# Optimization experiments

Measured on AMD Instinct MI355X. Metric: run time of the kernel, lower is better.

Reference implementation:

```python
import jax, jax.numpy as jnp
import numpy as np
from jax import lax

N_WIRES = 4
N_OPS = 30
BN_EPS = 1e-5


def _rl_ops():
    # Deterministic stand-in for tq.RandomLayer(n_ops=30): cycle rx/ry/rz/cnot.
    kinds = ['rx', 'ry', 'rz', 'cnot']
    ops, p = [], 0
    for i in range(N_OPS):
        k = kinds[i % 4]
        if k == 'cnot':
            ops.append((k, i % N_WIRES, (i + 1) % N_WIRES))
        else:
            ops.append((k, i % N_WIRES, p))
            p += 1
    return ops, p

RL_OPS, N_RL_PARAMS = _rl_ops()  # 23 rotation params, 7 cnots


def _rx(t):
    c = jnp.cos(t / 2).astype(jnp.complex64)
    s = (-1j * jnp.sin(t / 2).astype(jnp.complex64))
    return jnp.stack([jnp.stack([c, s], -1), jnp.stack([s, c], -1)], -2)


def _ry(t):
    c = jnp.cos(t / 2).astype(jnp.complex64)
    s = jnp.sin(t / 2).astype(jnp.complex64)
    return jnp.stack([jnp.stack([c, -s], -1), jnp.stack([s, c], -1)], -2)


def _rz(t):
    e = jnp.exp((-1j * t / 2).astype(jnp.complex64))
    z = jnp.zeros_like(e)
    return jnp.stack([jnp.stack([e, z], -1), jnp.stack([z, jnp.conj(e)], -1)], -2)


def _apply_1q(state, U, w):
    # state: [B,2,2,2,2]; U: [2,2] (shared) or [B,2,2] (per-sample)
    s = jnp.moveaxis(state, w + 1, -1)
    if U.ndim == 2:
        s = jnp.einsum('ij,b...j->b...i', U, s)
    else:
        s = jnp.einsum('bij,b...j->b...i', U, s)
    return jnp.moveaxis(s, -1, w + 1)


def _apply_cnot(state, c, t):
    s = jnp.moveaxis(state, (c + 1, t + 1), (-2, -1))
    s = s.at[..., 1, :].set(s[..., 1, ::-1])  # flip target where control==1
    return jnp.moveaxis(s, (-2, -1), (c + 1, t + 1))


# PauliZ expectation table: z[k, w] = +/-1 for basis state k on wire w
_ZTAB = np.array([[1.0 - 2.0 * ((k >> (N_WIRES - 1 - w)) & 1) for w in range(N_WIRES)]
                  for k in range(2 ** N_WIRES)], dtype=np.float32)  # [16,4]


def _conv(x, w, b):
    y = lax.conv_general_dilated(x, w, (1, 1), 'SAME',
                                 dimension_numbers=('NCHW', 'OIHW', 'NCHW'))
    return y + b[None, :, None, None]


def _maxpool2(x):
    return lax.reduce_window(x, -jnp.inf, lax.max, (1, 1, 2, 2), (1, 1, 2, 2), 'VALID')


def setup_inputs() -> dict:
    key = jax.random.key(0)
    ks = jax.random.split(key, 8)
    B = 8192
    return {
        'x': jax.random.normal(ks[0], (B, 1, 28, 28), jnp.float32),
        'conv1_w': jax.random.normal(ks[1], (8, 1, 3, 3), jnp.float32) * 0.1,
        'conv1_b': jnp.zeros((8,), jnp.float32),
        'conv2_w': jax.random.normal(ks[2], (16, 8, 3, 3), jnp.float32) * 0.1,
        'conv2_b': jnp.zeros((16,), jnp.float32),
        'fc1_w': jax.random.normal(ks[3], (64, 784), jnp.float32) * 0.05,
        'fc1_b': jnp.zeros((64,), jnp.float32),
        'fc2_w': jax.random.normal(ks[4], (4, 64), jnp.float32) * 0.1,
        'fc2_b': jnp.zeros((4,), jnp.float32),
        'bn_g': jnp.ones((4,), jnp.float32),
        'bn_b': jnp.zeros((4,), jnp.float32),
        'rl_params': jax.random.uniform(ks[5], (N_RL_PARAMS,), jnp.float32,
                                        -np.pi, np.pi),
    }


def reference(x, conv1_w, conv1_b, conv2_w, conv2_b, fc1_w, fc1_b,
              fc2_w, fc2_b, bn_g, bn_b, rl_params):
    B = x.shape[0]
    # CNN backbone: conv -> relu -> pool -> conv -> relu -> pool
    h = _maxpool2(jax.nn.relu(_conv(x, conv1_w, conv1_b)))          # [B,8,14,14]
    h = _maxpool2(jax.nn.relu(_conv(h, conv2_w, conv2_b)))          # [B,16,7,7]
    flat = h.reshape(B, -1)                                         # [B,784]
    h = jax.nn.relu(flat @ fc1_w.T + fc1_b)                         # [B,64]
    feat = h @ fc2_w.T + fc2_b                                      # [B,4]
    # BatchNorm1d (training mode: batch stats, biased variance)
    mean = feat.mean(0)
    var = feat.var(0)
    feat = (feat - mean) / jnp.sqrt(var + BN_EPS) * bn_g + bn_b
    # Quantum state-vector simulation on 4 wires, |0000> start
    state = jnp.zeros((B, 16), jnp.complex64).at[:, 0].set(1.0)
    state = state.reshape(B, 2, 2, 2, 2)
    # Encoder: RX(feat[:, w]) on wire w
    for w in range(N_WIRES):
        state = _apply_1q(state, _rx(feat[:, w]), w)
    # Random layer: 30 sequential gates with fixed trainable params
    gate_fns = {'rx': _rx, 'ry': _ry, 'rz': _rz}
    for kind, w, q in RL_OPS:
        if kind == 'cnot':
            state = _apply_cnot(state, w, q)
        else:
            state = _apply_1q(state, gate_fns[kind](rl_params[q]), w)
    # MeasureAll(PauliZ)
    probs = jnp.abs(state.reshape(B, 16)) ** 2                      # [B,16]
    return probs @ jnp.asarray(_ZTAB)                               # [B,4]
```

## Files before the change

kernel.cpp:

```cpp
#include <hip/hip_runtime.h>


#define B_EPS 1e-5f

typedef float f2 __attribute__((ext_vector_type(2)));

__device__ __forceinline__ f2 sp(float x)          { f2 r; r.x = x; r.y = x; return r; }
__device__ __forceinline__ f2 mk(float a, float b) { f2 r; r.x = a; r.y = b; return r; }
#define PKFMA(a, b, c) __builtin_elementwise_fma(a, b, c)
#define PKMAX(a, b)    __builtin_elementwise_max(a, b)

__device__ __forceinline__ void row_fma(f2* acc, const float* wp, const f2* rv)
{
    #pragma unroll
    for (int j = 0; j < 4; j++) {
        acc[j] = PKFMA(sp(wp[0]), rv[j],     acc[j]);
        acc[j] = PKFMA(sp(wp[1]), rv[j + 1], acc[j]);
        acc[j] = PKFMA(sp(wp[2]), rv[j + 2], acc[j]);
    }
}

__device__ __forceinline__ void load_rv6(f2* rv, const f2* rp)
{
    float4 A = *(const float4*)rp;
    float4 Bv = *(const float4*)(rp + 2);
    float4 Cv = *(const float4*)(rp + 4);
    rv[0] = mk(A.x, A.y);   rv[1] = mk(A.z, A.w);
    rv[2] = mk(Bv.x, Bv.y); rv[3] = mk(Bv.z, Bv.w);
    rv[4] = mk(Cv.x, Cv.y); rv[5] = mk(Cv.z, Cv.w);
}

__global__ void prep_kernel(const float* __restrict__ rl,
                            const float* __restrict__ f1w,
                            const float* __restrict__ c2w,
                            float* __restrict__ Uout,
                            float* __restrict__ wT2,
                            float* __restrict__ w2q,
                            float* __restrict__ stats)
{
    if (blockIdx.x == 0) {
        __shared__ float2 U[16][16];
        int t = threadIdx.x;
        int r = t >> 4, cc = t & 15;
        U[r][cc] = (r == cc) ? make_float2(1.f, 0.f) : make_float2(0.f, 0.f);
        stats[t] = 0.f;
        stats[t + 256] = 0.f;
        for (int i = t; i < 16 * 8 * 12; i += 256) {
            int ci = i / 192, rem = i - ci * 192;
            int c2 = rem / 12, qq = rem - c2 * 12;
            w2q[i] = (qq < 9) ? c2w[c2 * 72 + ci * 9 + qq] : 0.f;
        }
        __syncthreads();
        for (int op = 0; op < 30; op++) {
            int kind = op & 3;
            float2 cur = U[r][cc];
            float2 nv;
            if (kind == 3) {
                float2 part = U[r ^ 8][cc];
                nv = (r & 1) ? part : cur;
            } else {
                int m = 8 >> kind;
                float theta = rl[op - (op >> 2)];
                float ch = cosf(0.5f * theta), sh = sinf(0.5f * theta);
                float2 part = U[r ^ m][cc];
                int br = (r & m) ? 1 : 0;
                float2 gc, gp;
                if (kind == 0)      { gc = make_float2(ch, 0.f);           gp = make_float2(0.f, -sh); }
                else if (kind == 1) { gc = make_float2(ch, 0.f);           gp = make_float2(br ? sh : -sh, 0.f); }
                else                { gc = make_float2(ch, br ? sh : -sh); gp = make_float2(0.f, 0.f); }
                nv.x = gc.x*cur.x - gc.y*cur.y + gp.x*part.x - gp.y*part.y;
                nv.y = gc.x*cur.y + gc.y*cur.x + gp.x*part.y + gp.y*part.x;
            }
            __syncthreads();
            U[r][cc] = nv;
            __syncthreads();
        }
        ((float2*)Uout)[t] = U[r][cc];
    } else {
        int id = (blockIdx.x - 1) * 256 + threadIdx.x;
        if (id < 784 * 64) {
            int k = id >> 6, o = id & 63;
            wT2[(((k >> 2) * 64 + o) << 2) + (k & 3)] = f1w[o * 784 + k];
        }
    }
}

__global__ __launch_bounds__(256) void conv_kernel(
    const float* __restrict__ x,  const float* __restrict__ c1w,
    const float* __restrict__ c1b, const float* __restrict__ w2q,
    const float* __restrict__ c2b, const float* __restrict__ wT2,
    const float* __restrict__ f1b, const float* __restrict__ f2w,
    const float* __restrict__ f2bias, float* __restrict__ feat,
    float* __restrict__ stats)
{
    __shared__ union alignas(16) {
        f2 xin[30 * 32];
        f2 flat[784];
    } u;
    __shared__ union alignas(16) {
        f2 p1[8 * 290];
        struct { f2 part[4][64]; f2 hs[64]; } fc;
    } pu;

    int t = threadIdx.x;
    int w = t >> 6, lane = t & 63;

    int c1 = lane >> 3;
    float wk1[9];
    #pragma unroll
    for (int q = 0; q < 9; q++) wk1[q] = c1w[c1 * 9 + q];
    float bias1 = c1b[c1];

    {
        float4 z = make_float4(0.f, 0.f, 0.f, 0.f);
        float4* xz = (float4*)u.xin;
        for (int i = t; i < 480; i += 256) xz[i] = z;
        float4* pz = (float4*)pu.p1;
        for (int i = t; i < 1160; i += 256) pz[i] = z;
    }
    __syncthreads();

    {
        const float4* xg0 = (const float4*)(x + (size_t)blockIdx.x * 2 * 784);
        const float4* xg1 = xg0 + 196;
        if (t < 196) {
            float4 v0 = xg0[t];
            float4 v1 = xg1[t];
            int p = 4 * t, rr = p / 28, cb = p - rr * 28;
            f2* dst = &u.xin[(rr + 1) * 32 + cb + 3];
            dst[0] = mk(v0.x, v1.x);
            dst[1] = mk(v0.y, v1.y);
            dst[2] = mk(v0.z, v1.z);
            dst[3] = mk(v0.w, v1.w);
        }
    }
    __syncthreads();

    {
        int g = lane & 7;
        if (g < 7) {
            const f2* xb = &u.xin[4 * g + 2];
            f2* pout = &pu.p1[c1 * 290 + 3];
            #pragma unroll 1
            for (int k = 0; k < 4; k++) {
                int i = w + 4 * k;
                if (i > 13) break;
                f2 o_[2][4];
                #pragma unroll
                for (int dr = 0; dr < 2; dr++)
                    #pragma unroll
                    for (int j = 0; j < 4; j++) o_[dr][j] = sp(bias1);
                #pragma unroll
                for (int q = 0; q < 4; q++) {
                    f2 rv[6];
                    load_rv6(rv, xb + (2 * i + q) * 32);
                    if (q < 3)  row_fma(o_[0], &wk1[q * 3], rv);
                    if (q >= 1) row_fma(o_[1], &wk1[(q - 1) * 3], rv);
                }
                #pragma unroll
                for (int jj = 0; jj < 2; jj++) {
                    f2 m = PKMAX(PKMAX(o_[0][2 * jj], o_[0][2 * jj + 1]),
                                 PKMAX(o_[1][2 * jj], o_[1][2 * jj + 1]));
                    pout[(i + 1) * 18 + 2 * g + jj] = PKMAX(m, sp(0.f));
                }
            }
        }
    }
    __syncthreads();

    {
        int c2 = lane >> 2, g2 = lane & 3;
        float bias2 = c2b[c2];
        const float4* wqb = (const float4*)w2q + c2 * 3;
        #pragma unroll 1
        for (int k = 0; k < 2; k++) {
            int i = w + 4 * k;
            if (i > 6) break;
            f2 acc[2][4];
            #pragma unroll
            for (int dr = 0; dr < 2; dr++)
                #pragma unroll
                for (int j = 0; j < 4; j++) acc[dr][j] = sp(bias2);
            float4 wa = wqb[0], wb = wqb[1], wc = wqb[2];
            #pragma unroll 1
            for (int ci = 0; ci < 8; ci++) {
                float wk[9] = {wa.x, wa.y, wa.z, wa.w, wb.x, wb.y, wb.z, wb.w, wc.x};
                if (ci < 7) {
                    wa = wqb[(ci + 1) * 48];
                    wb = wqb[(ci + 1) * 48 + 1];
                    wc = wqb[(ci + 1) * 48 + 2];
                }
                const f2* pc_ = &pu.p1[ci * 290 + (2 * i) * 18 + 4 * g2 + 2];
                #pragma unroll
                for (int q = 0; q < 4; q++) {
                    f2 rv[6];
                    load_rv6(rv, pc_ + q * 18);
                    if (q < 3)  row_fma(acc[0], &wk[q * 3], rv);
                    if (q >= 1) row_fma(acc[1], &wk[(q - 1) * 3], rv);
                }
            }
            #pragma unroll
            for (int jj = 0; jj < 2; jj++) {
                int pc = 2 * g2 + jj;
                if (pc < 7) {
                    f2 m = PKMAX(PKMAX(acc[0][2 * jj], acc[0][2 * jj + 1]),
                                 PKMAX(acc[1][2 * jj], acc[1][2 * jj + 1]));
                    u.flat[c2 * 49 + i * 7 + pc] = PKMAX(m, sp(0.f));
                }
            }
        }
    }
    __syncthreads();

    {
        const f2* fl = u.flat;
        const float4* wp4 = (const float4*)wT2 + lane;
        int g0 = w * 49;
        f2 a0 = sp(0.f), a1 = sp(0.f);
        #pragma unroll 2
        for (int g = g0; g < g0 + 48; g += 2) {
            float4 wv0 = wp4[(size_t)g * 64];
            float4 wv1 = wp4[(size_t)(g + 1) * 64];
            float4 fA = *(const float4*)&fl[4 * g];
            float4 fB = *(const float4*)&fl[4 * g + 2];
            float4 fC = *(const float4*)&fl[4 * g + 4];
            float4 fD = *(const float4*)&fl[4 * g + 6];
            a0 = PKFMA(sp(wv0.x), mk(fA.x, fA.y), a0);
            a0 = PKFMA(sp(wv0.y), mk(fA.z, fA.w), a0);
            a0 = PKFMA(sp(wv0.z), mk(fB.x, fB.y), a0);
            a0 = PKFMA(sp(wv0.w), mk(fB.z, fB.w), a0);
            a1 = PKFMA(sp(wv1.x), mk(fC.x, fC.y), a1);
            a1 = PKFMA(sp(wv1.y), mk(fC.z, fC.w), a1);
            a1 = PKFMA(sp(wv1.z), mk(fD.x, fD.y), a1);
            a1 = PKFMA(sp(wv1.w), mk(fD.z, fD.w), a1);
        }
        {
            int g = g0 + 48;
            float4 wv = wp4[(size_t)g * 64];
            float4 fA = *(const float4*)&fl[4 * g];
            float4 fB = *(const float4*)&fl[4 * g + 2];
            a0 = PKFMA(sp(wv.x), mk(fA.x, fA.y), a0);
            a0 = PKFMA(sp(wv.y), mk(fA.z, fA.w), a0);
            a0 = PKFMA(sp(wv.z), mk(fB.x, fB.y), a0);
            a0 = PKFMA(sp(wv.w), mk(fB.z, fB.w), a0);
        }
        pu.fc.part[w][lane] = a0 + a1;
    }
    __syncthreads();

    if (t < 64) {
        f2 h = pu.fc.part[0][t] + pu.fc.part[1][t]
             + pu.fc.part[2][t] + pu.fc.part[3][t] + sp(f1b[t]);
        pu.fc.hs[t] = PKMAX(h, sp(0.f));
    }
    __syncthreads();

    if (t < 4) {
        int j = t;
        f2 a = sp(f2bias[j]);
        #pragma unroll
        for (int o = 0; o < 64; o++) a = PKFMA(sp(f2w[j * 64 + o]), pu.fc.hs[o], a);
        feat[((size_t)blockIdx.x * 2 + 0) * 4 + j] = a.x;
        feat[((size_t)blockIdx.x * 2 + 1) * 4 + j] = a.y;
        int g = blockIdx.x & 63;
        atomicAdd(&stats[g * 8 + j], a.x + a.y);
        atomicAdd(&stats[g * 8 + 4 + j], a.x * a.x + a.y * a.y);
    }
}

__global__ __launch_bounds__(128) void quantum_kernel(
    const float* __restrict__ feat, const float* __restrict__ Ug,
    const float* __restrict__ stats, const float* __restrict__ bn_g,
    const float* __restrict__ bn_b, float* __restrict__ out, int B)
{
    __shared__ float2 Us[256];
    __shared__ float sm[8];
    int t = threadIdx.x;
    for (int i = t; i < 256; i += 128) Us[i] = ((const float2*)Ug)[i];
    if (t < 8) sm[t] = 0.f;
    __syncthreads();
    {
        float v = stats[t] + stats[t + 128] + stats[t + 256] + stats[t + 384];
        atomicAdd(&sm[t & 7], v);
    }
    __syncthreads();
    int q = t & 3;
    int s = blockIdx.x * 32 + (t >> 2);
    float4 fv = ((const float4*)feat)[s];
    float f[4] = {fv.x, fv.y, fv.z, fv.w};
    float cn[4], sn[4];
    float invB = 1.0f / (float)B;
    #pragma unroll
    for (int w = 0; w < 4; w++) {
        float mean = sm[w] * invB;
        float var  = sm[4 + w] * invB - mean * mean;
        float fh = (f[w] - mean) / sqrtf(var + B_EPS) * bn_g[w] + bn_b[w];
        cn[w] = cosf(0.5f * fh);
        sn[w] = sinf(0.5f * fh);
    }
    float re0[16], im0[16];
    #pragma unroll
    for (int k = 0; k < 16; k++) {
        float mag = ((k & 8) ? sn[0] : cn[0]) * ((k & 4) ? sn[1] : cn[1]) *
                    ((k & 2) ? sn[2] : cn[2]) * ((k & 1) ? sn[3] : cn[3]);
        int m = __popc(k) & 3;
        re0[k] = (m == 0) ? mag : (m == 2) ? -mag : 0.f;
        im0[k] = (m == 1) ? -mag : (m == 3) ? mag : 0.f;
    }
    float o0 = 0.f, o1 = 0.f, o2 = 0.f, o3 = 0.f;
    #pragma unroll
    for (int i = 0; i < 4; i++) {
        int r = q * 4 + i;
        float ar = 0.f, ai = 0.f;
        #pragma unroll
        for (int k = 0; k < 16; k++) {
            float2 uu = Us[r * 16 + k];
            ar += uu.x * re0[k] - uu.y * im0[k];
            ai += uu.x * im0[k] + uu.y * re0[k];
        }
        float p = ar * ar + ai * ai;
        o0 += (r & 8) ? -p : p;
        o1 += (r & 4) ? -p : p;
        o2 += (r & 2) ? -p : p;
        o3 += (r & 1) ? -p : p;
    }
    o0 += __shfl_xor(o0, 1);  o0 += __shfl_xor(o0, 2);
    o1 += __shfl_xor(o1, 1);  o1 += __shfl_xor(o1, 2);
    o2 += __shfl_xor(o2, 1);  o2 += __shfl_xor(o2, 2);
    o3 += __shfl_xor(o3, 1);  o3 += __shfl_xor(o3, 2);
    if (q == 0) {
        float4 ov = {o0, o1, o2, o3};
        ((float4*)out)[s] = ov;
    }
}

extern "C" void kernel_launch(void* const* d_in, const int* in_sizes, int n_in,
                              void* d_out, int out_size, void* d_ws, size_t ws_size,
                              hipStream_t stream)
{
    const float* x   = (const float*)d_in[0];
    const float* c1w = (const float*)d_in[1];
    const float* c1b = (const float*)d_in[2];
    const float* c2w = (const float*)d_in[3];
    const float* c2b = (const float*)d_in[4];
    const float* f1w = (const float*)d_in[5];
    const float* f1b = (const float*)d_in[6];
    const float* f2w = (const float*)d_in[7];
    const float* f2b = (const float*)d_in[8];
    const float* bng = (const float*)d_in[9];
    const float* bnb = (const float*)d_in[10];
    const float* rl  = (const float*)d_in[11];
    float* out = (float*)d_out;

    int B = in_sizes[0] / 784;

    float* wsf   = (float*)d_ws;
    float* feat  = wsf;
    float* wT2   = feat + (size_t)B * 4;
    float* U     = wT2 + 784 * 64;
    float* stats = U + 512;
    float* w2q   = stats + 512;

    prep_kernel<<<197, 256, 0, stream>>>(rl, f1w, c2w, U, wT2, w2q, stats);
    conv_kernel<<<B / 2, 256, 0, stream>>>(x, c1w, c1b, w2q, c2b, wT2,
                                           f1b, f2w, f2b, feat, stats);
    quantum_kernel<<<B / 32, 128, 0, stream>>>(feat, U, stats, bng, bnb, out, B);
}
```

Baseline: 185.7 us.

## Compute two output channels per thread in conv1 and conv2 to reuse input loads

Each thread in conv1 and conv2 now accumulates two output channels from the same loaded input rows. This halves the shared-memory input reads per FMA, and the work is remapped across threads. Conv1 now gives each thread two rows with two channels. Conv2 now uses 224 threads, each covering one row with two channels, and loads its weights directly without prefetching. This raises register pressure and leaves 32 threads idle in conv2.

```diff
diff --git a/kernel.cpp b/kernel.cpp
--- a/kernel.cpp
+++ b/kernel.cpp
@@ -105,11 +105,15 @@
     int t = threadIdx.x;
     int w = t >> 6, lane = t & 63;
 
-    int c1 = lane >> 3;
-    float wk1[9];
-    #pragma unroll
-    for (int q = 0; q < 9; q++) wk1[q] = c1w[c1 * 9 + q];
-    float bias1 = c1b[c1];
+    int r2 = lane >> 5;
+    int p2p = (lane >> 3) & 3;
+    int g  = lane & 7;
+
+    int chA = 2 * p2p, chB = 2 * p2p + 1;
+    float wkA[9], wkB[9];
+    #pragma unroll
+    for (int q = 0; q < 9; q++) { wkA[q] = c1w[chA * 9 + q]; wkB[q] = c1w[chB * 9 + q]; }
+    float biasA = c1b[chA], biasB = c1b[chB];
 
     {
         float4 z = make_float4(0.f, 0.f, 0.f, 0.f);
@@ -126,7 +130,7 @@
         if (t < 196) {
             float4 v0 = xg0[t];
             float4 v1 = xg1[t];
-            int p = 4 * t, rr = p / 28, cb = p - rr * 28;
+            int pp = 4 * t, rr = pp / 28, cb = pp - rr * 28;
             f2* dst = &u.xin[(rr + 1) * 32 + cb + 3];
             dst[0] = mk(v0.x, v1.x);
             dst[1] = mk(v0.y, v1.y);
@@ -137,76 +141,84 @@
     __syncthreads();
 
     {
-        int g = lane & 7;
         if (g < 7) {
             const f2* xb = &u.xin[4 * g + 2];
-            f2* pout = &pu.p1[c1 * 290 + 3];
             #pragma unroll 1
-            for (int k = 0; k < 4; k++) {
-                int i = w + 4 * k;
+            for (int k = 0; k < 2; k++) {
+                int i = w * 2 + r2 + 8 * k;
                 if (i > 13) break;
-                f2 o_[2][4];
+                f2 oA[2][4], oB[2][4];
                 #pragma unroll
                 for (int dr = 0; dr < 2; dr++)
                     #pragma unroll
-                    for (int j = 0; j < 4; j++) o_[dr][j] = sp(bias1);
+                    for (int j = 0; j < 4; j++) { oA[dr][j] = sp(biasA); oB[dr][j] = sp(biasB); }
                 #pragma unroll
                 for (int q = 0; q < 4; q++) {
                     f2 rv[6];
                     load_rv6(rv, xb + (2 * i + q) * 32);
-                    if (q < 3)  row_fma(o_[0], &wk1[q * 3], rv);
-                    if (q >= 1) row_fma(o_[1], &wk1[(q - 1) * 3], rv);
+                    if (q < 3)  { row_fma(oA[0], &wkA[q * 3], rv);
+                                  row_fma(oB[0], &wkB[q * 3], rv); }
+                    if (q >= 1) { row_fma(oA[1], &wkA[(q - 1) * 3], rv);
+                                  row_fma(oB[1], &wkB[(q - 1) * 3], rv); }
                 }
+                f2* poutA = &pu.p1[chA * 290 + 3 + (i + 1) * 18 + 2 * g];
+                f2* poutB = &pu.p1[chB * 290 + 3 + (i + 1) * 18 + 2 * g];
                 #pragma unroll
                 for (int jj = 0; jj < 2; jj++) {
-                    f2 m = PKMAX(PKMAX(o_[0][2 * jj], o_[0][2 * jj + 1]),
-                                 PKMAX(o_[1][2 * jj], o_[1][2 * jj + 1]));
-                    pout[(i + 1) * 18 + 2 * g + jj] = PKMAX(m, sp(0.f));
+                    f2 mA = PKMAX(PKMAX(oA[0][2 * jj], oA[0][2 * jj + 1]),
+                                  PKMAX(oA[1][2 * jj], oA[1][2 * jj + 1]));
+                    f2 mB = PKMAX(PKMAX(oB[0][2 * jj], oB[0][2 * jj + 1]),
+                                  PKMAX(oB[1][2 * jj], oB[1][2 * jj + 1]));
+                    poutA[jj] = PKMAX(mA, sp(0.f));
+                    poutB[jj] = PKMAX(mB, sp(0.f));
                 }
             }
         }
     }
     __syncthreads();
 
-    {
-        int c2 = lane >> 2, g2 = lane & 3;
-        float bias2 = c2b[c2];
-        const float4* wqb = (const float4*)w2q + c2 * 3;
-        #pragma unroll 1
-        for (int k = 0; k < 2; k++) {
-            int i = w + 4 * k;
-            if (i > 6) break;
-            f2 acc[2][4];
+    if (t < 224) {
+        int i3  = t >> 5;
+        int p3  = (t >> 2) & 7;
+        int g2  = t & 3;
+        int cA = 2 * p3, cB = 2 * p3 + 1;
+        const float4* wqA = (const float4*)w2q + cA * 3;
+        const float4* wqB = (const float4*)w2q + cB * 3;
+        f2 accA[2][4], accB[2][4];
+        {
+            float bA = c2b[cA], bB = c2b[cB];
             #pragma unroll
             for (int dr = 0; dr < 2; dr++)
                 #pragma unroll
-                for (int j = 0; j < 4; j++) acc[dr][j] = sp(bias2);
-            float4 wa = wqb[0], wb = wqb[1], wc = wqb[2];
-            #pragma unroll 1
-            for (int ci = 0; ci < 8; ci++) {
-                float wk[9] = {wa.x, wa.y, wa.z, wa.w, wb.x, wb.y, wb.z, wb.w, wc.x};
-                if (ci < 7) {
-                    wa = wqb[(ci + 1) * 48];
-                    wb = wqb[(ci + 1) * 48 + 1];
-                    wc = wqb[(ci + 1) * 48 + 2];
-                }
-                const f2* pc_ = &pu.p1[ci * 290 + (2 * i) * 18 + 4 * g2 + 2];
-                #pragma unroll
-                for (int q = 0; q < 4; q++) {
-                    f2 rv[6];
-                    load_rv6(rv, pc_ + q * 18);
-                    if (q < 3)  row_fma(acc[0], &wk[q * 3], rv);
-                    if (q >= 1) row_fma(acc[1], &wk[(q - 1) * 3], rv);
-                }
+                for (int j = 0; j < 4; j++) { accA[dr][j] = sp(bA); accB[dr][j] = sp(bB); }
+        }
+        #pragma unroll 1
+        for (int ci = 0; ci < 8; ci++) {
+            float4 a0 = wqA[ci * 48], a1 = wqA[ci * 48 + 1], a2 = wqA[ci * 48 + 2];
+            float4 b0 = wqB[ci * 48], b1 = wqB[ci * 48 + 1], b2 = wqB[ci * 48 + 2];
+            float wA[9] = {a0.x, a0.y, a0.z, a0.w, a1.x, a1.y, a1.z, a1.w, a2.x};
+            float wB[9] = {b0.x, b0.y, b0.z, b0.w, b1.x, b1.y, b1.z, b1.w, b2.x};
+            const f2* pc_ = &pu.p1[ci * 290 + (2 * i3) * 18 + 4 * g2 + 2];
+            #pragma unroll
+            for (int q = 0; q < 4; q++) {
+                f2 rv[6];
+                load_rv6(rv, pc_ + q * 18);
+                if (q < 3)  { row_fma(accA[0], &wA[q * 3], rv);
+                              row_fma(accB[0], &wB[q * 3], rv); }
+                if (q >= 1) { row_fma(accA[1], &wA[(q - 1) * 3], rv);
+                              row_fma(accB[1], &wB[(q - 1) * 3], rv); }
             }
-            #pragma unroll
-            for (int jj = 0; jj < 2; jj++) {
-                int pc = 2 * g2 + jj;
-                if (pc < 7) {
-                    f2 m = PKMAX(PKMAX(acc[0][2 * jj], acc[0][2 * jj + 1]),
-                                 PKMAX(acc[1][2 * jj], acc[1][2 * jj + 1]));
-                    u.flat[c2 * 49 + i * 7 + pc] = PKMAX(m, sp(0.f));
-                }
+        }
+        #pragma unroll
+        for (int jj = 0; jj < 2; jj++) {
+            int pc = 2 * g2 + jj;
+            if (pc < 7) {
+                f2 mA = PKMAX(PKMAX(accA[0][2 * jj], accA[0][2 * jj + 1]),
+                              PKMAX(accA[1][2 * jj], accA[1][2 * jj + 1]));
+                f2 mB = PKMAX(PKMAX(accB[0][2 * jj], accB[0][2 * jj + 1]),
+                              PKMAX(accB[1][2 * jj], accB[1][2 * jj + 1]));
+                u.flat[cA * 49 + i3 * 7 + pc] = PKMAX(mA, sp(0.f));
+                u.flat[cB * 49 + i3 * 7 + pc] = PKMAX(mB, sp(0.f));
             }
         }
     }
@@ -218,13 +230,13 @@
         int g0 = w * 49;
         f2 a0 = sp(0.f), a1 = sp(0.f);
         #pragma unroll 2
-        for (int g = g0; g < g0 + 48; g += 2) {
-            float4 wv0 = wp4[(size_t)g * 64];
-            float4 wv1 = wp4[(size_t)(g + 1) * 64];
-            float4 fA = *(const float4*)&fl[4 * g];
-            float4 fB = *(const float4*)&fl[4 * g + 2];
-            float4 fC = *(const float4*)&fl[4 * g + 4];
-            float4 fD = *(const float4*)&fl[4 * g + 6];
+        for (int gg = g0; gg < g0 + 48; gg += 2) {
+            float4 wv0 = wp4[(size_t)gg * 64];
+            float4 wv1 = wp4[(size_t)(gg + 1) * 64];
+            float4 fA = *(const float4*)&fl[4 * gg];
+            float4 fB = *(const float4*)&fl[4 * gg + 2];
+            float4 fC = *(const float4*)&fl[4 * gg + 4];
+            float4 fD = *(const float4*)&fl[4 * gg + 6];
             a0 = PKFMA(sp(wv0.x), mk(fA.x, fA.y), a0);
             a0 = PKFMA(sp(wv0.y), mk(fA.z, fA.w), a0);
             a0 = PKFMA(sp(wv0.z), mk(fB.x, fB.y), a0);
@@ -235,10 +247,10 @@
             a1 = PKFMA(sp(wv1.w), mk(fD.z, fD.w), a1);
         }
         {
-            int g = g0 + 48;
-            float4 wv = wp4[(size_t)g * 64];
-            float4 fA = *(const float4*)&fl[4 * g];
-            float4 fB = *(const float4*)&fl[4 * g + 2];
+            int gg = g0 + 48;
+            float4 wv = wp4[(size_t)gg * 64];
+            float4 fA = *(const float4*)&fl[4 * gg];
+            float4 fB = *(const float4*)&fl[4 * gg + 2];
             a0 = PKFMA(sp(wv.x), mk(fA.x, fA.y), a0);
             a0 = PKFMA(sp(wv.y), mk(fA.z, fA.w), a0);
             a0 = PKFMA(sp(wv.z), mk(fB.x, fB.y), a0);
@@ -262,9 +274,9 @@
         for (int o = 0; o < 64; o++) a = PKFMA(sp(f2w[j * 64 + o]), pu.fc.hs[o], a);
         feat[((size_t)blockIdx.x * 2 + 0) * 4 + j] = a.x;
         feat[((size_t)blockIdx.x * 2 + 1) * 4 + j] = a.y;
-        int g = blockIdx.x & 63;
-        atomicAdd(&stats[g * 8 + j], a.x + a.y);
-        atomicAdd(&stats[g * 8 + 4 + j], a.x * a.x + a.y * a.y);
+        int g2 = blockIdx.x & 63;
+        atomicAdd(&stats[g2 * 8 + j], a.x + a.y);
+        atomicAdd(&stats[g2 * 8 + 4 + j], a.x * a.x + a.y * a.y);
     }
 }
 
@@ -318,11 +330,11 @@
             ar += uu.x * re0[k] - uu.y * im0[k];
             ai += uu.x * im0[k] + uu.y * re0[k];
         }
-        float p = ar * ar + ai * ai;
-        o0 += (r & 8) ? -p : p;
-        o1 += (r & 4) ? -p : p;
-        o2 += (r & 2) ? -p : p;
-        o3 += (r & 1) ? -p : p;
+        float pqr = ar * ar + ai * ai;
+        o0 += (r & 8) ? -pqr : pqr;
+        o1 += (r & 4) ? -pqr : pqr;
+        o2 += (r & 2) ? -pqr : pqr;
+        o3 += (r & 1) ? -pqr : pqr;
     }
     o0 += __shfl_xor(o0, 1);  o0 += __shfl_xor(o0, 2);
     o1 += __shfl_xor(o1, 1);  o1 += __shfl_xor(o1, 2);
```

Result: slower. 198.8 us (+7.1%).

## Process four samples per block so fc1 weights are shared across two pairs

Applied to the files above, without the earlier changes.

The conv kernel now runs 512 threads per block and handles two sample pairs, with the conv stages duplicated per pair in shared memory. In fc1, each weight float4 load from global memory now feeds both pairs, halving weight traffic per sample. The fc2 stage is spread across 128 threads and reduced with shuffles instead of 4 serial threads. Shared memory per block roughly doubles, which may reduce the number of resident blocks.

```diff
diff --git a/kernel.cpp b/kernel.cpp
--- a/kernel.cpp
+++ b/kernel.cpp
@@ -85,7 +85,7 @@
     }
 }
 
-__global__ __launch_bounds__(256) void conv_kernel(
+__global__ __launch_bounds__(512) void conv_kernel(
     const float* __restrict__ x,  const float* __restrict__ c1w,
     const float* __restrict__ c1b, const float* __restrict__ w2q,
     const float* __restrict__ c2b, const float* __restrict__ wT2,
@@ -94,16 +94,17 @@
     float* __restrict__ stats)
 {
     __shared__ union alignas(16) {
-        f2 xin[30 * 32];
-        f2 flat[784];
+        f2 xin[2][30 * 32];
+        f2 flat[2][784];
     } u;
     __shared__ union alignas(16) {
-        f2 p1[8 * 290];
-        struct { f2 part[4][64]; f2 hs[64]; } fc;
+        f2 p1[2][8 * 290];
+        struct { f2 part[8][2][64]; f2 hs[2][64]; } fc;
     } pu;
 
     int t = threadIdx.x;
-    int w = t >> 6, lane = t & 63;
+    int w8 = t >> 6, lane = t & 63;
+    int pair = w8 >> 2, wp = w8 & 3;
 
     int c1 = lane >> 3;
     float wk1[9];
@@ -114,20 +115,20 @@
     {
         float4 z = make_float4(0.f, 0.f, 0.f, 0.f);
         float4* xz = (float4*)u.xin;
-        for (int i = t; i < 480; i += 256) xz[i] = z;
+        for (int i = t; i < 960; i += 512) xz[i] = z;
         float4* pz = (float4*)pu.p1;
-        for (int i = t; i < 1160; i += 256) pz[i] = z;
-    }
-    __syncthreads();
-
-    {
-        const float4* xg0 = (const float4*)(x + (size_t)blockIdx.x * 2 * 784);
-        const float4* xg1 = xg0 + 196;
-        if (t < 196) {
-            float4 v0 = xg0[t];
-            float4 v1 = xg1[t];
-            int p = 4 * t, rr = p / 28, cb = p - rr * 28;
-            f2* dst = &u.xin[(rr + 1) * 32 + cb + 3];
+        for (int i = t; i < 2320; i += 512) pz[i] = z;
+    }
+    __syncthreads();
+
+    {
+        const float4* xg = (const float4*)(x + (size_t)blockIdx.x * 4 * 784);
+        if (t < 392) {
+            int pr = t / 196, tt = t - pr * 196;
+            float4 v0 = xg[(2 * pr) * 196 + tt];
+            float4 v1 = xg[(2 * pr + 1) * 196 + tt];
+            int p = 4 * tt, rr = p / 28, cb = p - rr * 28;
+            f2* dst = &u.xin[pr][(rr + 1) * 32 + cb + 3];
             dst[0] = mk(v0.x, v1.x);
             dst[1] = mk(v0.y, v1.y);
             dst[2] = mk(v0.z, v1.z);
@@ -139,11 +140,11 @@
     {
         int g = lane & 7;
         if (g < 7) {
-            const f2* xb = &u.xin[4 * g + 2];
-            f2* pout = &pu.p1[c1 * 290 + 3];
+            const f2* xb = &u.xin[pair][4 * g + 2];
+            f2* pout = &pu.p1[pair][c1 * 290 + 3];
             #pragma unroll 1
             for (int k = 0; k < 4; k++) {
-                int i = w + 4 * k;
+                int i = wp + 4 * k;
                 if (i > 13) break;
                 f2 o_[2][4];
                 #pragma unroll
@@ -174,7 +175,7 @@
         const float4* wqb = (const float4*)w2q + c2 * 3;
         #pragma unroll 1
         for (int k = 0; k < 2; k++) {
-            int i = w + 4 * k;
+            int i = wp + 4 * k;
             if (i > 6) break;
             f2 acc[2][4];
             #pragma unroll
@@ -190,7 +191,7 @@
                     wb = wqb[(ci + 1) * 48 + 1];
                     wc = wqb[(ci + 1) * 48 + 2];
                 }
-                const f2* pc_ = &pu.p1[ci * 290 + (2 * i) * 18 + 4 * g2 + 2];
+                const f2* pc_ = &pu.p1[pair][ci * 290 + (2 * i) * 18 + 4 * g2 + 2];
                 #pragma unroll
                 for (int q = 0; q < 4; q++) {
                     f2 rv[6];
@@ -205,7 +206,7 @@
                 if (pc < 7) {
                     f2 m = PKMAX(PKMAX(acc[0][2 * jj], acc[0][2 * jj + 1]),
                                  PKMAX(acc[1][2 * jj], acc[1][2 * jj + 1]));
-                    u.flat[c2 * 49 + i * 7 + pc] = PKMAX(m, sp(0.f));
+                    u.flat[pair][c2 * 49 + i * 7 + pc] = PKMAX(m, sp(0.f));
                 }
             }
         }
@@ -213,58 +214,62 @@
     __syncthreads();
 
     {
-        const f2* fl = u.flat;
+        const f2* flA = u.flat[0];
+        const f2* flB = u.flat[1];
         const float4* wp4 = (const float4*)wT2 + lane;
-        int g0 = w * 49;
         f2 a0 = sp(0.f), a1 = sp(0.f);
         #pragma unroll 2
-        for (int g = g0; g < g0 + 48; g += 2) {
-            float4 wv0 = wp4[(size_t)g * 64];
-            float4 wv1 = wp4[(size_t)(g + 1) * 64];
-            float4 fA = *(const float4*)&fl[4 * g];
-            float4 fB = *(const float4*)&fl[4 * g + 2];
-            float4 fC = *(const float4*)&fl[4 * g + 4];
-            float4 fD = *(const float4*)&fl[4 * g + 6];
-            a0 = PKFMA(sp(wv0.x), mk(fA.x, fA.y), a0);
-            a0 = PKFMA(sp(wv0.y), mk(fA.z, fA.w), a0);
-            a0 = PKFMA(sp(wv0.z), mk(fB.x, fB.y), a0);
-            a0 = PKFMA(sp(wv0.w), mk(fB.z, fB.w), a0);
-            a1 = PKFMA(sp(wv1.x), mk(fC.x, fC.y), a1);
-            a1 = PKFMA(sp(wv1.y), mk(fC.z, fC.w), a1);
-            a1 = PKFMA(sp(wv1.z), mk(fD.x, fD.y), a1);
-            a1 = PKFMA(sp(wv1.w), mk(fD.z, fD.w), a1);
-        }
-        {
-            int g = g0 + 48;
+        for (int g = w8; g < 196; g += 8) {
             float4 wv = wp4[(size_t)g * 64];
-            float4 fA = *(const float4*)&fl[4 * g];
-            float4 fB = *(const float4*)&fl[4 * g + 2];
+            float4 fA = *(const float4*)&flA[4 * g];
+            float4 fB = *(const float4*)&flA[4 * g + 2];
+            float4 fC = *(const float4*)&flB[4 * g];
+            float4 fD = *(const float4*)&flB[4 * g + 2];
             a0 = PKFMA(sp(wv.x), mk(fA.x, fA.y), a0);
             a0 = PKFMA(sp(wv.y), mk(fA.z, fA.w), a0);
             a0 = PKFMA(sp(wv.z), mk(fB.x, fB.y), a0);
             a0 = PKFMA(sp(wv.w), mk(fB.z, fB.w), a0);
-        }
-        pu.fc.part[w][lane] = a0 + a1;
-    }
-    __syncthreads();
-
-    if (t < 64) {
-        f2 h = pu.fc.part[0][t] + pu.fc.part[1][t]
-             + pu.fc.part[2][t] + pu.fc.part[3][t] + sp(f1b[t]);
-        pu.fc.hs[t] = PKMAX(h, sp(0.f));
-    }
-    __syncthreads();
-
-    if (t < 4) {
-        int j = t;
-        f2 a = sp(f2bias[j]);
+            a1 = PKFMA(sp(wv.x), mk(fC.x, fC.y), a1);
+            a1 = PKFMA(sp(wv.y), mk(fC.z, fC.w), a1);
+            a1 = PKFMA(sp(wv.z), mk(fD.x, fD.y), a1);
+            a1 = PKFMA(sp(wv.w), mk(fD.z, fD.w), a1);
+        }
+        pu.fc.part[w8][0][lane] = a0;
+        pu.fc.part[w8][1][lane] = a1;
+    }
+    __syncthreads();
+
+    if (t < 128) {
+        int p = t >> 6, o = t & 63;
+        f2 h = pu.fc.part[0][p][o] + pu.fc.part[1][p][o]
+             + pu.fc.part[2][p][o] + pu.fc.part[3][p][o]
+             + pu.fc.part[4][p][o] + pu.fc.part[5][p][o]
+             + pu.fc.part[6][p][o] + pu.fc.part[7][p][o] + sp(f1b[o]);
+        pu.fc.hs[p][o] = PKMAX(h, sp(0.f));
+    }
+    __syncthreads();
+
+    if (t < 128) {
+        int p = t >> 6, tt = t & 63;
+        int j = tt >> 4, ob = (tt & 15) * 4;
+        f2 a = sp(0.f);
         #pragma unroll
-        for (int o = 0; o < 64; o++) a = PKFMA(sp(f2w[j * 64 + o]), pu.fc.hs[o], a);
-        feat[((size_t)blockIdx.x * 2 + 0) * 4 + j] = a.x;
-        feat[((size_t)blockIdx.x * 2 + 1) * 4 + j] = a.y;
-        int g = blockIdx.x & 63;
-        atomicAdd(&stats[g * 8 + j], a.x + a.y);
-        atomicAdd(&stats[g * 8 + 4 + j], a.x * a.x + a.y * a.y);
+        for (int o = 0; o < 4; o++)
+            a = PKFMA(sp(f2w[j * 64 + ob + o]), pu.fc.hs[p][ob + o], a);
+        #pragma unroll
+        for (int m = 1; m < 16; m <<= 1) {
+            a.x += __shfl_xor(a.x, m);
+            a.y += __shfl_xor(a.y, m);
+        }
+        if ((tt & 15) == 0) {
+            a += sp(f2bias[j]);
+            size_t s0 = (size_t)blockIdx.x * 4 + 2 * p;
+            feat[s0 * 4 + j]       = a.x;
+            feat[(s0 + 1) * 4 + j] = a.y;
+            int g = blockIdx.x & 63;
+            atomicAdd(&stats[g * 8 + j], a.x + a.y);
+            atomicAdd(&stats[g * 8 + 4 + j], a.x * a.x + a.y * a.y);
+        }
     }
 }
 
@@ -362,7 +367,7 @@
     float* w2q   = stats + 512;
 
     prep_kernel<<<197, 256, 0, stream>>>(rl, f1w, c2w, U, wT2, w2q, stats);
-    conv_kernel<<<B / 2, 256, 0, stream>>>(x, c1w, c1b, w2q, c2b, wT2,
+    conv_kernel<<<B / 4, 512, 0, stream>>>(x, c1w, c1b, w2q, c2b, wT2,
                                            f1b, f2w, f2b, feat, stats);
     quantum_kernel<<<B / 32, 128, 0, stream>>>(feat, U, stats, bng, bnb, out, B);
 }
```

Result: faster. 181.9 us, median of 2 (-2.1%).
